# Kernel tuning notes

Measured on AMD Instinct MI355X. Metric: run time of the kernel, lower is better.

The kernel has to match this reference:

```python
import jax, jax.numpy as jnp
import numpy as np
from jax import lax

B, S, V, E, H = 64, 512, 50000, 300, 256


def _run_lstm(x, w_ih, w_hh, b_ih, b_hh, reverse):
    # x: [B,S,D]; w_ih: [4H,D]; w_hh: [4H,H]. PyTorch gate order: i,f,g,o.
    gx = jnp.einsum('bsd,gd->sbg', x, w_ih) + b_ih + b_hh  # [S,B,4H]
    Hh = w_hh.shape[1]

    def step(carry, g):
        h, c = carry
        g = g + h @ w_hh.T
        i, f, gg, o = jnp.split(g, 4, axis=-1)
        c = jax.nn.sigmoid(f) * c + jax.nn.sigmoid(i) * jnp.tanh(gg)
        h = jax.nn.sigmoid(o) * jnp.tanh(c)
        return (h, c), h

    init = (jnp.zeros((x.shape[0], Hh), x.dtype), jnp.zeros((x.shape[0], Hh), x.dtype))
    _, hs = lax.scan(step, init, gx, reverse=reverse)  # outputs aligned to input time order
    return jnp.swapaxes(hs, 0, 1)  # [B,S,H]


def _bilstm(x, wif, whf, bif, bhf, wib, whb, bib, bhb):
    fwd = _run_lstm(x, wif, whf, bif, bhf, False)
    bwd = _run_lstm(x, wib, whb, bib, bhb, True)
    return jnp.concatenate([fwd, bwd], axis=-1)  # [B,S,2H]


def setup_inputs() -> dict:
    key = jax.random.key(0)
    ks = iter(jax.random.split(key, 32))
    k = 1.0 / np.sqrt(H)
    u = lambda shape: jax.random.uniform(next(ks), shape, jnp.float32, -k, k)
    inp = {
        'input_ids': jax.random.randint(next(ks), (B, S), 0, V),
        'labels': jax.random.uniform(next(ks), (B, S), jnp.float32),
        'input_masks': jnp.ones((B, S), jnp.int64),
        'emb': jax.random.normal(next(ks), (V, E), jnp.float32) * 0.1,
    }
    # layer 0 (input E), layer 1 (input 2H); forward and backward directions
    for layer, d_in in ((0, E), (1, 2 * H)):
        for direc in ('f', 'b'):
            inp[f'w_ih_l{layer}{direc}'] = u((4 * H, d_in))
            inp[f'w_hh_l{layer}{direc}'] = u((4 * H, H))
            inp[f'b_ih_l{layer}{direc}'] = u((4 * H,))
            inp[f'b_hh_l{layer}{direc}'] = u((4 * H,))
    inp['w_lin'] = u((H,))
    inp['b_lin'] = u(())
    return inp


def reference(input_ids, labels, input_masks, emb,
              w_ih_l0f, w_hh_l0f, b_ih_l0f, b_hh_l0f,
              w_ih_l0b, w_hh_l0b, b_ih_l0b, b_hh_l0b,
              w_ih_l1f, w_hh_l1f, b_ih_l1f, b_hh_l1f,
              w_ih_l1b, w_hh_l1b, b_ih_l1b, b_hh_l1b,
              w_lin, b_lin):
    x = emb[input_ids]  # one-shot gather, replaces the double python loop: [B,S,E]
    h1 = _bilstm(x, w_ih_l0f, w_hh_l0f, b_ih_l0f, b_hh_l0f,
                 w_ih_l0b, w_hh_l0b, b_ih_l0b, b_hh_l0b)
    h2 = _bilstm(h1, w_ih_l1f, w_hh_l1f, b_ih_l1f, b_hh_l1f,
                 w_ih_l1b, w_hh_l1b, b_ih_l1b, b_hh_l1b)  # [B,S,2H]
    b, s = h2.shape[0], h2.shape[1]
    mean_dir = h2.reshape(b, s, 2, H).mean(axis=2)  # mean over directions
    scores = jax.nn.sigmoid(jnp.einsum('bsh,h->bs', mean_dir, w_lin) + b_lin)
    mask = input_masks.astype(scores.dtype)
    err = (scores - labels) ** 2 * mask
    loss = jnp.mean(jnp.sum(err, axis=1) / jnp.sum(mask, axis=1))
    return scores, loss
```

## Files before the change

kernel.cpp:

```cpp
#include <hip/hip_runtime.h>
#include <hip/hip_bf16.h>
#include <stdint.h>

#define B_  64
#define S_  512
#define E_  300
#define H_  256
#define T_  (B_*S_)
#define G4H 1024

using half8  = __attribute__((ext_vector_type(8))) _Float16;
using half4  = __attribute__((ext_vector_type(4))) _Float16;
using float4v = __attribute__((ext_vector_type(4))) float;

union H2 { _Float16 h[2]; uint32_t u; };

__device__ inline float sigm(float x) { return 1.f / (1.f + __expf(-x)); }
__device__ inline float tanhf_(float x) {
  float cx = fminf(fmaxf(x, -15.f), 15.f);
  float e = __expf(2.f * cx);
  return (e - 1.f) / (e + 1.f);
}

#define BARRIER() asm volatile("s_waitcnt lgkmcnt(0)\n\ts_barrier" ::: "memory")

__device__ inline void ld3_sc0(const uint64_t* p0, const uint64_t* p1,
                               const uint64_t* p2, uint4& a, uint4& b, uint4& c) {
  asm volatile(
      "global_load_dwordx4 %0, %3, off sc0\n\t"
      "global_load_dwordx4 %1, %4, off sc0\n\t"
      "global_load_dwordx4 %2, %5, off sc0\n\t"
      "s_waitcnt vmcnt(0)"
      : "=&v"(a), "=&v"(b), "=&v"(c)
      : "v"(p0), "v"(p1), "v"(p2) : "memory");
}
__device__ inline void st_sc0(uint64_t* p, uint64_t v) {
  asm volatile("global_store_dwordx2 %0, %1, off sc0" :: "v"(p), "v"(v) : "memory");
}
__device__ inline uint4 ldx4_pin(const _Float16* p) {
  uint4 r;
  asm volatile("global_load_dwordx4 %0, %1, off\n\ts_waitcnt vmcnt(0)"
               : "=v"(r) : "v"(p));
  return r;
}

__global__ __launch_bounds__(256) void k_prep_wih(const float* __restrict__ wf,
    const float* __restrict__ wb, _Float16* __restrict__ Bt,
    int KIN, int KP, int total)
{
  int idx = blockIdx.x * 256 + threadIdx.x;
  if (idx >= total) return;
  int n = idx / KP, k = idx % KP;
  int dd = n >> 10, nn = n & 1023;
  int row = (nn & 3) * 256 + (nn >> 2);
  const float* src = dd ? wb : wf;
  Bt[idx] = (_Float16)(k < KIN ? src[row * KIN + k] : 0.f);
}

__global__ __launch_bounds__(256) void k_prep_whh(const float* __restrict__ wf,
    const float* __restrict__ wb, _Float16* __restrict__ Wr)
{
  int idx = blockIdx.x * 256 + threadIdx.x;
  int dd = idx >> 18;
  int rem = idx & 262143;
  int n = rem >> 8, k = rem & 255;
  int row = (n & 3) * 256 + (n >> 2);
  Wr[idx] = (_Float16)((dd ? wb : wf)[row * 256 + k]);
}

__global__ void k_prep_bias(const float* __restrict__ bif, const float* __restrict__ bhf,
    const float* __restrict__ bib, const float* __restrict__ bhb, float* __restrict__ bias)
{
  int n = blockIdx.x * 256 + threadIdx.x;
  int dd = n >> 10, nn = n & 1023;
  int row = (nn & 3) * 256 + (nn >> 2);
  bias[n] = dd ? (bib[row] + bhb[row]) : (bif[row] + bhf[row]);
}

__global__ __launch_bounds__(256) void k_gather(const int* __restrict__ ids,
    const float* __restrict__ emb, _Float16* __restrict__ xbf)
{
  int idx = blockIdx.x * 256 + threadIdx.x;
  int tt = idx / 40;
  int ch = idx % 40;
  int b = tt & 63, s = tt >> 6;
  int id = ids[b * S_ + s];
  const float* src = emb + (size_t)id * E_ + ch * 8;
  half8 v;
#pragma unroll
  for (int e = 0; e < 8; ++e) {
    int k = ch * 8 + e;
    v[e] = (_Float16)(k < E_ ? src[e] : 0.f);
  }
  *(half8*)(xbf + (size_t)tt * 320 + ch * 8) = v;
}

template<int K>
__global__ __launch_bounds__(256) void k_gemm(const _Float16* __restrict__ A,
    const _Float16* __restrict__ Bt, const float* __restrict__ bias,
    _Float16* __restrict__ gx)
{
  __shared__ _Float16 sA[128 * 72];
  __shared__ _Float16 sB[128 * 72];
  const int tid = threadIdx.x;
  const int t0 = blockIdx.y * 128;
  const int n0 = blockIdx.x * 128;
  const int lane = tid & 63, wid = tid >> 6;
  const int l15 = lane & 15, q = lane >> 4;
  const int wm = wid & 1, wn = wid >> 1;

  float4v acc[4][4] = {};

  for (int kt = 0; kt < K / 64; ++kt) {
    __syncthreads();
#pragma unroll
    for (int c = 0; c < 4; ++c) {
      int f = tid * 4 + c;
      int row = f >> 3, seg = f & 7;
      *(half8*)&sA[row * 72 + seg * 8] =
          *(const half8*)(A + (size_t)(t0 + row) * K + kt * 64 + seg * 8);
      *(half8*)&sB[row * 72 + seg * 8] =
          *(const half8*)(Bt + (size_t)(n0 + row) * K + kt * 64 + seg * 8);
    }
    __syncthreads();
#pragma unroll
    for (int kk = 0; kk < 2; ++kk) {
      half8 a[4], b[4];
#pragma unroll
      for (int mt = 0; mt < 4; ++mt)
        a[mt] = *(const half8*)&sA[(wm * 64 + mt * 16 + l15) * 72 + kk * 32 + q * 8];
#pragma unroll
      for (int nt = 0; nt < 4; ++nt)
        b[nt] = *(const half8*)&sB[(wn * 64 + nt * 16 + l15) * 72 + kk * 32 + q * 8];
#pragma unroll
      for (int mt = 0; mt < 4; ++mt)
#pragma unroll
        for (int nt = 0; nt < 4; ++nt)
          acc[mt][nt] = __builtin_amdgcn_mfma_f32_16x16x32_f16(a[mt], b[nt], acc[mt][nt], 0, 0, 0);
    }
  }

#pragma unroll
  for (int mt = 0; mt < 4; ++mt) {
#pragma unroll
    for (int nt = 0; nt < 4; ++nt) {
      int token = t0 + wm * 64 + mt * 16 + q * 4;
      int n = n0 + wn * 64 + nt * 16 + l15;
      float bs = bias[n];
      size_t base = (size_t)(n >> 10) * ((size_t)T_ * G4H) + (size_t)token * G4H + (n & 1023);
#pragma unroll
      for (int r = 0; r < 4; ++r)
        gx[base + (size_t)r * G4H] = (_Float16)(acc[mt][nt][r] + bs);
    }
  }
}

template<int LAYER>
__global__ __launch_bounds__(256, 1) void k_rec(const _Float16* __restrict__ gx,
    const _Float16* __restrict__ Wr, uint64_t* __restrict__ hxf,
    uint64_t* __restrict__ hxs, _Float16* __restrict__ h1bf,
    float* __restrict__ pd2, const float* __restrict__ w_lin)
{
  const int bx = blockIdx.x;
  const int cg = bx & 7, rg = bx >> 3;
  const int d = cg >> 2, g = cg & 3;
  const int tid = threadIdx.x;
  const int lane = tid & 63, wv = tid >> 6;
  const int l15 = lane & 15, q = lane >> 4;
  const int b0g = g * 16;
  const int n0g = rg * 256;

  __shared__ _Float16 hstage[16 * 288];
  __shared__ float    preS[16 * 260];

  for (int i = tid; i < 16 * 144; i += 256)
    ((uint32_t*)hstage)[i] = 0u;

  uint4 wreg[4][8];
#pragma unroll
  for (int nt = 0; nt < 4; ++nt)
#pragma unroll
    for (int kt = 0; kt < 8; ++kt)
      wreg[nt][kt] = ldx4_pin(Wr +
          (size_t)(d * G4H + n0g + wv * 64 + nt * 16 + l15) * H_ + kt * 32 + q * 8);

  const int bl = tid >> 4;
  const int jl4 = (tid & 15) * 4;
  const int bglob = b0g + bl;
  const int jg = rg * 64 + jl4;
  float wl[4];
#pragma unroll
  for (int cc = 0; cc < 4; ++cc) wl[cc] = w_lin[jg + cc];
  float creg[4] = {0.f, 0.f, 0.f, 0.f};

  uint64_t* fbase = hxf + (size_t)cg * 2 * 2048;
  uint64_t* sbase = hxs + (size_t)cg * 2 * 2048;
  const int off2 = tid * 2;
  const int q2a = (rg + 1) & 3, q2b = (rg + 2) & 3, q2c = (rg + 3) & 3;

  half8 gxa, gxb;
  {
    const int time0 = d ? (S_ - 1) : 0;
    const _Float16* gp = gx + ((size_t)d * T_ + (size_t)time0 * B_ + bglob) * G4H
                           + n0g + (tid & 15) * 16;
    gxa = *(const half8*)(gp);
    gxb = *(const half8*)(gp + 8);
  }

  for (int t = 0; t < S_; ++t) {
    const int time = d ? (S_ - 1 - t) : t;

    if (t > 0) {
      const uint64_t* fs = fbase + (size_t)(t & 1) * 2048;
      const uint64_t* ss = sbase + (size_t)(t & 1) * 2048;
      const uint32_t tt = (uint32_t)t;
      uint32_t dat[6];
      unsigned pend = 0x3fu;
      int round = 0;
      while (pend) {
        uint4 A, Bv, C;
        ld3_sc0(fs + q2a * 512 + off2, fs + q2b * 512 + off2,
                fs + q2c * 512 + off2, A, Bv, C);
        if ((pend & 1u)  && A.y  == tt) { dat[0] = A.x;  pend &= ~1u; }
        if ((pend & 2u)  && A.w  == tt) { dat[1] = A.z;  pend &= ~2u; }
        if ((pend & 4u)  && Bv.y == tt) { dat[2] = Bv.x; pend &= ~4u; }
        if ((pend & 8u)  && Bv.w == tt) { dat[3] = Bv.z; pend &= ~8u; }
        if ((pend & 16u) && C.y  == tt) { dat[4] = C.x;  pend &= ~16u; }
        if ((pend & 32u) && C.w  == tt) { dat[5] = C.z;  pend &= ~32u; }
        if (pend && ((++round & 3) == 0)) {
          const int wq[3] = {q2a, q2b, q2c};
#pragma unroll
          for (int k3 = 0; k3 < 3; ++k3)
#pragma unroll
            for (int j = 0; j < 2; ++j) {
              int w = k3 * 2 + j;
              if (pend & (1u << w)) {
                uint64_t v = __hip_atomic_load(ss + wq[k3] * 512 + off2 + j,
                                               __ATOMIC_RELAXED, __HIP_MEMORY_SCOPE_AGENT);
                if ((uint32_t)(v >> 32) == tt) { dat[w] = (uint32_t)v; pend &= ~(1u << w); }
              }
            }
        }
      }
      const int sb = tid >> 4, jp = (tid & 15) * 2;
      uint2 va; va.x = dat[0]; va.y = dat[1];
      uint2 vb; vb.x = dat[2]; vb.y = dat[3];
      uint2 vc; vc.x = dat[4]; vc.y = dat[5];
      *(uint2*)&((uint32_t*)hstage)[sb * 144 + q2a * 32 + jp] = va;
      *(uint2*)&((uint32_t*)hstage)[sb * 144 + q2b * 32 + jp] = vb;
      *(uint2*)&((uint32_t*)hstage)[sb * 144 + q2c * 32 + jp] = vc;
    }
    BARRIER();

    half8 gxa_n, gxb_n;
    {
      const int tn = (t + 1 < S_) ? t + 1 : t;
      const int timen = d ? (S_ - 1 - tn) : tn;
      const _Float16* gp = gx + ((size_t)d * T_ + (size_t)timen * B_ + bglob) * G4H
                             + n0g + (tid & 15) * 16;
      gxa_n = *(const half8*)(gp);
      gxb_n = *(const half8*)(gp + 8);
    }

    float4v acc[4] = {};
#pragma unroll
    for (int kt = 0; kt < 8; ++kt) {
      half8 a = *(const half8*)&hstage[l15 * 288 + kt * 32 + q * 8];
#pragma unroll
      for (int nt = 0; nt < 4; ++nt)
        acc[nt] = __builtin_amdgcn_mfma_f32_16x16x32_f16(
            a, __builtin_bit_cast(half8, wreg[nt][kt]), acc[nt], 0, 0, 0);
    }
#pragma unroll
    for (int nt = 0; nt < 4; ++nt)
#pragma unroll
      for (int r = 0; r < 4; ++r)
        preS[(q * 4 + r) * 260 + wv * 64 + nt * 16 + l15] = acc[nt][r];
    BARRIER();

    half4 hv4;
    float partial = 0.f;
#pragma unroll
    for (int cc = 0; cc < 4; ++cc) {
      float4v p = *(const float4v*)&preS[bl * 260 + (jl4 + cc) * 4];
      float gxi = (float)(cc < 2 ? gxa[cc * 4 + 0] : gxb[(cc - 2) * 4 + 0]);
      float gxf = (float)(cc < 2 ? gxa[cc * 4 + 1] : gxb[(cc - 2) * 4 + 1]);
      float gxg = (float)(cc < 2 ? gxa[cc * 4 + 2] : gxb[(cc - 2) * 4 + 2]);
      float gxo = (float)(cc < 2 ? gxa[cc * 4 + 3] : gxb[(cc - 2) * 4 + 3]);
      float gi = p[0] + gxi, gf = p[1] + gxf, gg = p[2] + gxg, go = p[3] + gxo;
      float cv = sigm(gf) * creg[cc] + sigm(gi) * tanhf_(gg);
      float hv = sigm(go) * tanhf_(cv);
      creg[cc] = cv;
      hv4[cc] = (_Float16)hv;
      if (LAYER == 1) partial += 0.5f * hv * wl[cc];
    }

    {
      H2 p0; p0.h[0] = hv4[0]; p0.h[1] = hv4[1];
      H2 p1; p1.h[0] = hv4[2]; p1.h[1] = hv4[3];
      uint32_t tg = (uint32_t)(t + 1);
      uint64_t w0 = ((uint64_t)tg << 32) | p0.u;
      uint64_t w1 = ((uint64_t)tg << 32) | p1.u;
      uint64_t* fd = fbase + (size_t)((t + 1) & 1) * 2048 + rg * 512 + off2;
      st_sc0(fd + 0, w0);
      st_sc0(fd + 1, w1);
      uint64_t* sd = sbase + (size_t)((t + 1) & 1) * 2048 + rg * 512 + off2;
      __hip_atomic_store(sd + 0, w0, __ATOMIC_RELAXED, __HIP_MEMORY_SCOPE_AGENT);
      __hip_atomic_store(sd + 1, w1, __ATOMIC_RELAXED, __HIP_MEMORY_SCOPE_AGENT);
    }

    *(half4*)&hstage[bl * 288 + jg] = hv4;

    if (LAYER == 0) {
      *(half4*)(h1bf + ((size_t)time * B_ + bglob) * 512 + d * H_ + jg) = hv4;
    } else {
      partial += __shfl_xor(partial, 1);
      partial += __shfl_xor(partial, 2);
      partial += __shfl_xor(partial, 4);
      partial += __shfl_xor(partial, 8);
      if ((tid & 15) == 0)
        atomicAdd(pd2 + ((size_t)d * B_ + bglob) * S_ + time, partial);
    }

    gxa = gxa_n; gxb = gxb_n;
  }
}

__global__ __launch_bounds__(256) void k_final(const float* __restrict__ pd2,
    const float* __restrict__ labels, const int* __restrict__ masks,
    const float* __restrict__ b_lin, float* __restrict__ out)
{
  int b = blockIdx.x;
  int tid = threadIdx.x;
  float bl = b_lin[0];
  float se = 0.f, sm = 0.f;
  for (int s = tid; s < S_; s += 256) {
    float p = pd2[(size_t)b * S_ + s] + pd2[(size_t)(B_ + b) * S_ + s];
    float sc = sigm(p + bl);
    out[b * S_ + s] = sc;
    float m = (float)masks[b * S_ + s];
    float e = sc - labels[b * S_ + s];
    se += e * e * m;
    sm += m;
  }
  for (int off = 1; off < 64; off <<= 1) {
    se += __shfl_xor(se, off);
    sm += __shfl_xor(sm, off);
  }
  __shared__ float rs[4], rm[4];
  int wid = tid >> 6;
  if ((tid & 63) == 0) { rs[wid] = se; rm[wid] = sm; }
  __syncthreads();
  if (tid == 0) {
    float te = 0.f, tm = 0.f;
    for (int w = 0; w < 4; ++w) { te += rs[w]; tm += rm[w]; }
    atomicAdd(out + T_, (te / tm) * (1.f / 64.f));
  }
}

extern "C" void kernel_launch(void* const* d_in, const int* in_sizes, int n_in,
                              void* d_out, int out_size, void* d_ws, size_t ws_size,
                              hipStream_t stream)
{
  (void)in_sizes; (void)n_in; (void)out_size; (void)ws_size;
  const int*   ids    = (const int*)d_in[0];
  const float* labels = (const float*)d_in[1];
  const int*   masks  = (const int*)d_in[2];
  const float* emb    = (const float*)d_in[3];
  const float* w_ih_0f = (const float*)d_in[4];
  const float* w_hh_0f = (const float*)d_in[5];
  const float* b_ih_0f = (const float*)d_in[6];
  const float* b_hh_0f = (const float*)d_in[7];
  const float* w_ih_0b = (const float*)d_in[8];
  const float* w_hh_0b = (const float*)d_in[9];
  const float* b_ih_0b = (const float*)d_in[10];
  const float* b_hh_0b = (const float*)d_in[11];
  const float* w_ih_1f = (const float*)d_in[12];
  const float* w_hh_1f = (const float*)d_in[13];
  const float* b_ih_1f = (const float*)d_in[14];
  const float* b_hh_1f = (const float*)d_in[15];
  const float* w_ih_1b = (const float*)d_in[16];
  const float* w_hh_1b = (const float*)d_in[17];
  const float* b_ih_1b = (const float*)d_in[18];
  const float* b_hh_1b = (const float*)d_in[19];
  const float* w_lin   = (const float*)d_in[20];
  const float* b_lin   = (const float*)d_in[21];
  float* out = (float*)d_out;

  char* ws = (char*)d_ws;
  size_t off = 0;
  auto alloc = [&](size_t bytes) -> char* {
    char* p = ws + off;
    off += (bytes + 255) & ~(size_t)255;
    return p;
  };
  _Float16* xbf   = (_Float16*)alloc((size_t)T_ * 320 * 2);
  _Float16* h1bf  = (_Float16*)alloc((size_t)T_ * 512 * 2);
  _Float16* gx    = (_Float16*)alloc((size_t)2 * T_ * G4H * 2);
  _Float16* Bt0   = (_Float16*)alloc((size_t)2048 * 320 * 2);
  _Float16* Bt1   = (_Float16*)alloc((size_t)2048 * 512 * 2);
  _Float16* Wr0   = (_Float16*)alloc((size_t)2 * G4H * H_ * 2);
  _Float16* Wr1   = (_Float16*)alloc((size_t)2 * G4H * H_ * 2);
  float*    bias0 = (float*)alloc(2048 * 4);
  float*    bias1 = (float*)alloc(2048 * 4);
  uint64_t* hxf0  = (uint64_t*)alloc((size_t)8 * 2 * 2048 * 8);
  uint64_t* hxs0  = (uint64_t*)alloc((size_t)8 * 2 * 2048 * 8);
  uint64_t* hxf1  = (uint64_t*)alloc((size_t)8 * 2 * 2048 * 8);
  uint64_t* hxs1  = (uint64_t*)alloc((size_t)8 * 2 * 2048 * 8);
  float*    pd2   = (float*)alloc((size_t)2 * B_ * S_ * 4);

  k_prep_wih<<<(2048 * 320) / 256, 256, 0, stream>>>(w_ih_0f, w_ih_0b, Bt0, 300, 320, 2048 * 320);
  k_prep_wih<<<(2048 * 512) / 256, 256, 0, stream>>>(w_ih_1f, w_ih_1b, Bt1, 512, 512, 2048 * 512);
  k_prep_whh<<<524288 / 256, 256, 0, stream>>>(w_hh_0f, w_hh_0b, Wr0);
  k_prep_whh<<<524288 / 256, 256, 0, stream>>>(w_hh_1f, w_hh_1b, Wr1);
  k_prep_bias<<<8, 256, 0, stream>>>(b_ih_0f, b_hh_0f, b_ih_0b, b_hh_0b, bias0);
  k_prep_bias<<<8, 256, 0, stream>>>(b_ih_1f, b_hh_1f, b_ih_1b, b_hh_1b, bias1);
  k_gather<<<(T_ * 40) / 256, 256, 0, stream>>>(ids, emb, xbf);

  hipMemsetAsync(hxf0, 0, (size_t)8 * 2 * 2048 * 8, stream);
  hipMemsetAsync(hxs0, 0, (size_t)8 * 2 * 2048 * 8, stream);
  hipMemsetAsync(hxf1, 0, (size_t)8 * 2 * 2048 * 8, stream);
  hipMemsetAsync(hxs1, 0, (size_t)8 * 2 * 2048 * 8, stream);
  hipMemsetAsync(pd2, 0, (size_t)2 * B_ * S_ * 4, stream);
  hipMemsetAsync((char*)d_out + (size_t)T_ * 4, 0, 4, stream);

  k_gemm<320><<<dim3(16, 256), 256, 0, stream>>>(xbf, Bt0, bias0, gx);
  k_rec<0><<<32, 256, 0, stream>>>(gx, Wr0, hxf0, hxs0, h1bf, pd2, w_lin);

  k_gemm<512><<<dim3(16, 256), 256, 0, stream>>>(h1bf, Bt1, bias1, gx);
  k_rec<1><<<32, 256, 0, stream>>>(gx, Wr1, hxf1, hxs1, h1bf, pd2, w_lin);

  k_final<<<64, 256, 0, stream>>>(pd2, labels, masks, b_lin, out);
}
```

Before: 3.328 ms.

## Assign recurrent-kernel roles by XCD so each column group shares one die

The recurrent kernel now launches 256 blocks. Each block reads its hardware XCC id and atomically claims one of four slots on that die, so the four row-groups of each column group land on the same XCD and their cross-block h exchange stays within one L2. Extra blocks exit, and a fallback loop rebalances roles onto dies that are short of blocks. This is meant to cut cross-die coherence latency in the per-timestep synchronisation, at the cost of launching extra blocks and adding a spin-based claiming phase.

```diff
diff --git a/kernel.cpp b/kernel.cpp
--- a/kernel.cpp
+++ b/kernel.cpp
@@ -43,6 +43,11 @@
                : "=v"(r) : "v"(p));
   return r;
 }
+__device__ inline int xcc_id() {
+  int x;
+  asm volatile("s_getreg_b32 %0, hwreg(HW_REG_XCC_ID, 0, 32)" : "=s"(x));
+  return x & 7;
+}
 
 __global__ __launch_bounds__(256) void k_prep_wih(const float* __restrict__ wf,
     const float* __restrict__ wb, _Float16* __restrict__ Bt,
@@ -159,12 +164,45 @@
 __global__ __launch_bounds__(256, 1) void k_rec(const _Float16* __restrict__ gx,
     const _Float16* __restrict__ Wr, uint64_t* __restrict__ hxf,
     uint64_t* __restrict__ hxs, _Float16* __restrict__ h1bf,
-    float* __restrict__ pd2, const float* __restrict__ w_lin)
-{
-  const int bx = blockIdx.x;
-  const int cg = bx & 7, rg = bx >> 3;
+    float* __restrict__ pd2, const float* __restrict__ w_lin,
+    int* __restrict__ claim)
+{
+  const int tid = threadIdx.x;
+  __shared__ int role_sh;
+
+  if (tid == 0) {
+    int xcd = xcc_id();
+    int slot = __hip_atomic_fetch_add(claim + xcd, 1, __ATOMIC_RELAXED,
+                                      __HIP_MEMORY_SCOPE_AGENT);
+    int role = -1;
+    if (slot < 4) {
+      role = xcd * 4 + slot;
+    } else {
+      for (int it = 0;; ++it) {
+        int s = 0, deficit = -1;
+        for (int x = 0; x < 8; ++x) {
+          int v = __hip_atomic_load(claim + x, __ATOMIC_RELAXED,
+                                    __HIP_MEMORY_SCOPE_AGENT);
+          s += (v < 4 ? v : 4);
+          if (v < 4) deficit = x;
+        }
+        if (s == 32) break;
+        if (it > 8 && deficit >= 0) {
+          int r = __hip_atomic_fetch_add(claim + deficit, 1, __ATOMIC_RELAXED,
+                                         __HIP_MEMORY_SCOPE_AGENT);
+          if (r < 4) { role = deficit * 4 + r; break; }
+        }
+        __builtin_amdgcn_s_sleep(64);
+      }
+    }
+    role_sh = role;
+  }
+  __syncthreads();
+  const int role = role_sh;
+  if (role < 0) return;
+
+  const int cg = role >> 2, rg = role & 3;
   const int d = cg >> 2, g = cg & 3;
-  const int tid = threadIdx.x;
   const int lane = tid & 63, wv = tid >> 6;
   const int l15 = lane & 15, q = lane >> 4;
   const int b0g = g * 16;
@@ -408,6 +446,8 @@
   uint64_t* hxf1  = (uint64_t*)alloc((size_t)8 * 2 * 2048 * 8);
   uint64_t* hxs1  = (uint64_t*)alloc((size_t)8 * 2 * 2048 * 8);
   float*    pd2   = (float*)alloc((size_t)2 * B_ * S_ * 4);
+  int*      claim0 = (int*)alloc(256);
+  int*      claim1 = (int*)alloc(256);
 
   k_prep_wih<<<(2048 * 320) / 256, 256, 0, stream>>>(w_ih_0f, w_ih_0b, Bt0, 300, 320, 2048 * 320);
   k_prep_wih<<<(2048 * 512) / 256, 256, 0, stream>>>(w_ih_1f, w_ih_1b, Bt1, 512, 512, 2048 * 512);
@@ -422,13 +462,15 @@
   hipMemsetAsync(hxf1, 0, (size_t)8 * 2 * 2048 * 8, stream);
   hipMemsetAsync(hxs1, 0, (size_t)8 * 2 * 2048 * 8, stream);
   hipMemsetAsync(pd2, 0, (size_t)2 * B_ * S_ * 4, stream);
+  hipMemsetAsync(claim0, 0, 256, stream);
+  hipMemsetAsync(claim1, 0, 256, stream);
   hipMemsetAsync((char*)d_out + (size_t)T_ * 4, 0, 4, stream);
 
   k_gemm<320><<<dim3(16, 256), 256, 0, stream>>>(xbf, Bt0, bias0, gx);
-  k_rec<0><<<32, 256, 0, stream>>>(gx, Wr0, hxf0, hxs0, h1bf, pd2, w_lin);
+  k_rec<0><<<256, 256, 0, stream>>>(gx, Wr0, hxf0, hxs0, h1bf, pd2, w_lin, claim0);
 
   k_gemm<512><<<dim3(16, 256), 256, 0, stream>>>(h1bf, Bt1, bias1, gx);
-  k_rec<1><<<32, 256, 0, stream>>>(gx, Wr1, hxf1, hxs1, h1bf, pd2, w_lin);
+  k_rec<1><<<256, 256, 0, stream>>>(gx, Wr1, hxf1, hxs1, h1bf, pd2, w_lin, claim1);
 
   k_final<<<64, 256, 0, stream>>>(pd2, labels, masks, b_lin, out);
 }
```

After: 3.297 ms. No clear change (-0.9%).
